# Kernel optimization log

Measured on AMD Instinct MI355X. Metric: run time of the kernel, lower is better.

## Reference

```python
import jax, jax.numpy as jnp
import numpy as np
from jax import lax

B, S, T = 32, 128, 128
V_SRC, V_TGT, E, U = 32000, 32000, 128, 256


def _lstm(xs, h0, c0, Wx, Wh, b):
    # xs: [T, B, F]; Keras gate order i, f, g(candidate), o
    def step(carry, x):
        h, c = carry
        z = x @ Wx + h @ Wh + b
        i, f, g, o = jnp.split(z, 4, axis=-1)
        c = jax.nn.sigmoid(f) * c + jax.nn.sigmoid(i) * jnp.tanh(g)
        h = jax.nn.sigmoid(o) * jnp.tanh(c)
        return (h, c), h
    (h, c), hs = lax.scan(step, (h0, c0), xs)
    return hs, h, c


def setup_inputs() -> dict:
    key = jax.random.key(0)
    ks = jax.random.split(key, 20)
    p = lambda k, shp: (jax.random.normal(k, shp, dtype=jnp.float32) * 0.02)
    return {
        "src": jax.random.randint(ks[0], (B, S), 0, V_SRC),
        "tgt": jax.random.randint(ks[1], (B, T), 0, V_TGT),
        "enc_emb": p(ks[2], (V_SRC, E)),
        "enc_Wx": p(ks[3], (E, 4 * U)),
        "enc_Wh": p(ks[4], (U, 4 * U)),
        "enc_b": jnp.zeros((4 * U,), jnp.float32),
        "dec_emb": p(ks[5], (V_TGT, E)),
        "dec_Wx": p(ks[6], (U + E, 4 * U)),
        "dec_Wh": p(ks[7], (U, 4 * U)),
        "dec_b": jnp.zeros((4 * U,), jnp.float32),
        "att_W1": p(ks[8], (U, U)),
        "att_b1": jnp.zeros((U,), jnp.float32),
        "att_W2": p(ks[9], (U, U)),
        "att_b2": jnp.zeros((U,), jnp.float32),
        "att_V": p(ks[10], (U, 1)),
        "att_bV": jnp.zeros((1,), jnp.float32),
        "fc_W": p(ks[11], (U, V_TGT)),
        "fc_b": jnp.zeros((V_TGT,), jnp.float32),
    }


def reference(src, tgt, enc_emb, enc_Wx, enc_Wh, enc_b, dec_emb, dec_Wx, dec_Wh,
              dec_b, att_W1, att_b1, att_W2, att_b2, att_V, att_bV, fc_W, fc_b):
    # ---- encoder ----
    enc_x = enc_emb[src]                                  # [B,S,E]
    enc_hs, h, c = _lstm(enc_x.transpose(1, 0, 2),
                         jnp.zeros((B, U), enc_Wx.dtype),
                         jnp.zeros((B, U), enc_Wx.dtype),
                         enc_Wx, enc_Wh, enc_b)
    enc_out = enc_hs.transpose(1, 0, 2)                   # [B,S,U]
    keys = enc_out @ att_W2 + att_b2                      # [B,S,U] (hoisted, same math)

    # ---- decoder (faithful: step 0 uses tgt[:,0]; step t>=1 uses tgt[:,t-1]) ----
    dec_tokens = jnp.concatenate([tgt[:, :1], tgt[:, :-1]], axis=1)  # [B,T]
    dec_x = dec_emb[dec_tokens].transpose(1, 0, 2)        # [T,B,E]

    def step(carry, x_emb):
        h, c = carry
        q = (h @ att_W1 + att_b1)[:, None, :]             # [B,1,U]
        score = jnp.tanh(q + keys) @ att_V + att_bV       # [B,S,1]
        attn = jax.nn.softmax(score, axis=1)
        ctx = jnp.sum(attn * enc_out, axis=1)             # [B,U]
        xin = jnp.concatenate([ctx, x_emb], axis=-1)      # [B,U+E]
        z = xin @ dec_Wx + h @ dec_Wh + dec_b
        i, f, g, o = jnp.split(z, 4, axis=-1)
        c = jax.nn.sigmoid(f) * c + jax.nn.sigmoid(i) * jnp.tanh(g)
        h = jax.nn.sigmoid(o) * jnp.tanh(c)
        probs = jax.nn.softmax(h @ fc_W + fc_b, axis=-1)  # [B,V]
        return (h, c), probs

    _, out = lax.scan(step, (h, c), dec_x)                # [T,B,V]
    return out.transpose(1, 0, 2)                         # [B,T,V]
```

## Files before the change

kernel.cpp:

```cpp
#include <hip/hip_runtime.h>
#include <hip/hip_bf16.h>
#include <hip/hip_fp16.h>
#include <cstdint>
#include <cstddef>

#define B_ 32
#define S_ 128
#define T_ 128
#define E_ 128
#define U_ 256
#define V_ 32000
#define G4 1024
#define TV 4096000

typedef __attribute__((ext_vector_type(8))) short short8_t;
typedef __attribute__((ext_vector_type(4))) float f32x4;
typedef unsigned long long u64;

static __device__ __forceinline__ unsigned short f2bf(float x) {
  union { float f; unsigned int u; } v; v.f = x;
  unsigned int r = (v.u + 0x7fffu + ((v.u >> 16) & 1u)) >> 16;
  return (unsigned short)r;
}
static __device__ __forceinline__ unsigned int pack2bf(float a, float b) {
  return (unsigned int)f2bf(a) | ((unsigned int)f2bf(b) << 16);
}
static __device__ __forceinline__ float bf_lo(unsigned int w) { return __uint_as_float(w << 16); }
static __device__ __forceinline__ float bf_hi(unsigned int w) { return __uint_as_float(w & 0xffff0000u); }
static __device__ __forceinline__ float sigmoidf_(float x) {
  return 1.0f / (1.0f + __expf(-x));
}
static __device__ __forceinline__ float tanhf_(float x) {
  float e = __expf(2.0f * x);
  return 1.0f - 2.0f / (e + 1.0f);
}

static __device__ __forceinline__ unsigned int f2e5(float x) {
  __half h = __float2half(x);
  __half_raw hr = *(__half_raw*)&h;
  unsigned int u = hr.x;
  unsigned int r = (u + 0x7Fu + ((u >> 8) & 1u)) >> 8;
  return r & 0xFFu;
}

static __device__ __forceinline__ unsigned pk2(float a, float b) {
  auto h = __builtin_amdgcn_cvt_pkrtz(a, b);
  return __builtin_bit_cast(unsigned, h);
}
#define SEL01 0x05000400u
#define SEL23 0x07000600u
static __device__ __forceinline__ unsigned e5pair(unsigned w, unsigned sel) {
  return __builtin_amdgcn_perm(w, 0u, sel);
}
static __device__ __forceinline__ float dot2(unsigned a, unsigned b, float c) {
  float d;
  asm("v_dot2_f32_f16 %0, %1, %2, %3" : "=v"(d) : "v"(a), "v"(b), "v"(c));
  return d;
}
static __device__ __forceinline__ unsigned pkadd(unsigned a, unsigned b) {
  unsigned d; asm("v_pk_add_f16 %0, %1, %2" : "=v"(d) : "v"(a), "v"(b)); return d;
}
static __device__ __forceinline__ unsigned pkmul(unsigned a, unsigned b) {
  unsigned d; asm("v_pk_mul_f16 %0, %1, %2" : "=v"(d) : "v"(a), "v"(b)); return d;
}
static __device__ __forceinline__ unsigned pkfma(unsigned a, unsigned b, unsigned c) {
  unsigned d; asm("v_pk_fma_f16 %0, %1, %2, %3" : "=v"(d) : "v"(a), "v"(b), "v"(c)); return d;
}
static __device__ __forceinline__ unsigned pkmax(unsigned a, unsigned b) {
  unsigned d; asm("v_pk_max_f16 %0, %1, %2" : "=v"(d) : "v"(a), "v"(b)); return d;
}
static __device__ __forceinline__ unsigned pkmin(unsigned a, unsigned b) {
  unsigned d; asm("v_pk_min_f16 %0, %1, %2" : "=v"(d) : "v"(a), "v"(b)); return d;
}

static __device__ __forceinline__ void pub64u(u64* p, unsigned val, unsigned tag) {
  u64 v = ((u64)tag << 32) | (u64)val;
  __hip_atomic_store(p, v, __ATOMIC_RELAXED, __HIP_MEMORY_SCOPE_AGENT);
}
static __device__ __forceinline__ void pub64(u64* p, float val, unsigned tag) {
  pub64u(p, __float_as_uint(val), tag);
}
static __device__ __forceinline__ u64 ld64(const u64* p) {
  return __hip_atomic_load(p, __ATOMIC_RELAXED, __HIP_MEMORY_SCOPE_AGENT);
}

__global__ __launch_bounds__(256) void k_prep_x(
    const int* __restrict__ src, const int* __restrict__ tgt,
    const float* __restrict__ enc_emb, const float* __restrict__ enc_Wx,
    const float* __restrict__ enc_b,
    const float* __restrict__ dec_emb, const float* __restrict__ dec_Wx,
    const float* __restrict__ dec_b,
    float* __restrict__ Xe, float* __restrict__ Xd)
{
  __shared__ float emb_l[8][E_];
  int wg = blockIdx.x;
  int tid = threadIdx.x;
  bool is_dec = (wg >= 512);
  int r0 = (is_dec ? (wg - 512) : wg) * 8;
  const float* emb  = is_dec ? dec_emb : enc_emb;
  const float* W    = is_dec ? (dec_Wx + (size_t)U_ * G4) : enc_Wx;
  const float* bias = is_dec ? dec_b : enc_b;
  float* Xout = is_dec ? Xd : Xe;

  for (int i = 0; i < 4; ++i) {
    int lin = i * 256 + tid;
    int rr = lin >> 7, k = lin & 127;
    int r = r0 + rr;
    int b = r & 31, st = r >> 5;
    int tok;
    if (is_dec) tok = tgt[b * T_ + (st > 0 ? st - 1 : 0)];
    else        tok = src[b * S_ + st];
    emb_l[rr][k] = emb[(size_t)tok * E_ + k];
  }
  __syncthreads();

  float acc[8][4];
  #pragma unroll
  for (int rr = 0; rr < 8; ++rr)
    #pragma unroll
    for (int cc = 0; cc < 4; ++cc) acc[rr][cc] = 0.f;

  for (int k = 0; k < E_; ++k) {
    float w0 = W[(size_t)k * G4 + tid];
    float w1 = W[(size_t)k * G4 + tid + 256];
    float w2 = W[(size_t)k * G4 + tid + 512];
    float w3 = W[(size_t)k * G4 + tid + 768];
    #pragma unroll
    for (int rr = 0; rr < 8; ++rr) {
      float e = emb_l[rr][k];
      acc[rr][0] += e * w0; acc[rr][1] += e * w1;
      acc[rr][2] += e * w2; acc[rr][3] += e * w3;
    }
  }
  #pragma unroll
  for (int rr = 0; rr < 8; ++rr) {
    int r = r0 + rr;
    #pragma unroll
    for (int cc = 0; cc < 4; ++cc) {
      int col = tid + cc * 256;
      Xout[(size_t)r * G4 + col] = acc[rr][cc] + bias[col];
    }
  }
}

__global__ __launch_bounds__(256) void k_prep_fcw(
    const float* __restrict__ fcW, unsigned short* __restrict__ fcWt)
{
  __shared__ float tile[64][65];
  int bid = blockIdx.x, tid = threadIdx.x;
  int n0 = (bid % 500) * 64, k0 = (bid / 500) * 64;
  for (int i = 0; i < 16; ++i) {
    int lin = i * 256 + tid;
    int k = lin >> 6, n = lin & 63;
    tile[k][n] = fcW[(size_t)(k0 + k) * V_ + n0 + n];
  }
  __syncthreads();
  for (int i = 0; i < 16; ++i) {
    int lin = i * 256 + tid;
    int n = lin >> 6, k = lin & 63;
    fcWt[(size_t)(n0 + n) * 256 + k0 + k] = f2bf(tile[k][n]);
  }
}

__global__ __launch_bounds__(256) void k_encoder8(
    const float* __restrict__ Xe, const float* __restrict__ Wh,
    float* __restrict__ enc_out, float* __restrict__ h_state,
    float* __restrict__ c_state, u64* __restrict__ hpubE )
{
  __shared__ unsigned int WhL[128][128];
  __shared__ float h_l[256];
  __shared__ float zp[2][128];

  int bid = blockIdx.x, tid = threadIdx.x;
  int g = bid & 7, b = bid >> 3;

  {
    int cl = tid & 127, kh = tid >> 7;
    int q = cl >> 5, r = cl & 31;
    int gc = q * 256 + g * 32 + r;
    for (int k2 = kh; k2 < 128; k2 += 2) {
      float w0 = Wh[(size_t)(2 * k2) * G4 + gc];
      float w1 = Wh[(size_t)(2 * k2 + 1) * G4 + gc];
      WhL[k2][cl] = pack2bf(w0, w1);
    }
  }
  float c_reg = 0.f, h_reg = 0.f;
  __syncthreads();

  for (int s = 0; s < S_; ++s) {
    if (s == 0) {
      h_l[tid] = 0.f;
    } else {
      const u64* p = &hpubE[((size_t)(s & 1) * 32 + b) * 256 + tid];
      u64 v = ld64(p);
      while ((unsigned)(v >> 32) < (unsigned)s) { __builtin_amdgcn_s_sleep(1); v = ld64(p); }
      h_l[tid] = __uint_as_float((unsigned)v);
    }
    __syncthreads();
    {
      int half = tid >> 7, cl = tid & 127;
      int k2b = half * 64;
      float a0 = 0.f, a1 = 0.f, a2 = 0.f, a3 = 0.f;
      #pragma unroll 4
      for (int k2 = 0; k2 < 64; k2 += 4) {
        unsigned w0 = WhL[k2b + k2][cl];
        unsigned w1 = WhL[k2b + k2 + 1][cl];
        unsigned w2 = WhL[k2b + k2 + 2][cl];
        unsigned w3 = WhL[k2b + k2 + 3][cl];
        a0 += h_l[2*(k2b+k2)]   * bf_lo(w0) + h_l[2*(k2b+k2)+1] * bf_hi(w0);
        a1 += h_l[2*(k2b+k2)+2] * bf_lo(w1) + h_l[2*(k2b+k2)+3] * bf_hi(w1);
        a2 += h_l[2*(k2b+k2)+4] * bf_lo(w2) + h_l[2*(k2b+k2)+5] * bf_hi(w2);
        a3 += h_l[2*(k2b+k2)+6] * bf_lo(w3) + h_l[2*(k2b+k2)+7] * bf_hi(w3);
      }
      zp[half][cl] = (a0 + a1) + (a2 + a3);
    }
    __syncthreads();
    if (tid < 32) {
      int r = tid, gc = g * 32 + r;
      const float* xe = Xe + (size_t)(s * B_ + b) * G4;
      float zi = zp[0][r]      + zp[1][r]      + xe[gc];
      float zf = zp[0][32 + r] + zp[1][32 + r] + xe[256 + gc];
      float zg = zp[0][64 + r] + zp[1][64 + r] + xe[512 + gc];
      float zo = zp[0][96 + r] + zp[1][96 + r] + xe[768 + gc];
      float c = sigmoidf_(zf) * c_reg + sigmoidf_(zi) * tanhf_(zg);
      c_reg = c;
      float h = sigmoidf_(zo) * tanhf_(c);
      h_reg = h;
      enc_out[((size_t)(b * S_ + s)) * U_ + gc] = h;
      pub64(&hpubE[((size_t)((s + 1) & 1) * 32 + b) * 256 + gc], h, (unsigned)(s + 1));
    }
  }
  if (tid < 32) {
    h_state[b * U_ + g * 32 + tid] = h_reg;
    c_state[b * U_ + g * 32 + tid] = c_reg;
  }
}

__global__ __launch_bounds__(256) void k_keys(
    const float* __restrict__ enc_out, const float* __restrict__ W2,
    const float* __restrict__ b2, float* __restrict__ keys)
{
  __shared__ float x_l[8][U_];
  int wg = blockIdx.x, tid = threadIdx.x;
  int r0 = wg * 8;
  for (int i = 0; i < 8; ++i) x_l[i][tid] = enc_out[(size_t)(r0 + i) * U_ + tid];
  __syncthreads();
  float acc[8];
  #pragma unroll
  for (int rr = 0; rr < 8; ++rr) acc[rr] = 0.f;
  for (int k = 0; k < U_; ++k) {
    float w = W2[(size_t)k * U_ + tid];
    #pragma unroll
    for (int rr = 0; rr < 8; ++rr) acc[rr] += x_l[rr][k] * w;
  }
  float bb = b2[tid];
  #pragma unroll
  for (int rr = 0; rr < 8; ++rr)
    keys[(size_t)(r0 + rr) * U_ + tid] = acc[rr] + bb;
}

__global__ __launch_bounds__(512) void k_decoder8(
    const float* __restrict__ Xd, const float* __restrict__ dec_Wx,
    const float* __restrict__ Wh,
    const float* __restrict__ W1, const float* __restrict__ b1,
    const float* __restrict__ attV, const float* __restrict__ attbV,
    const float* __restrict__ enc_out, const float* __restrict__ keys,
    const float* __restrict__ h0, const float* __restrict__ c0,
    unsigned short* __restrict__ Hbf,
    u64* __restrict__ hpub2 ,
    u64* __restrict__ qp2   )
{
  __shared__ unsigned int WxU[128 * 65];
  __shared__ unsigned int WhU[128 * 65];
  __shared__ unsigned int keyU[128 * 65];
  __shared__ unsigned int eoT[256 * 33];
  __shared__ unsigned int W1L[16][256];
  __shared__ unsigned int q2[160];
  __shared__ unsigned int aV2[160];
  __shared__ unsigned int b1p[128];
  __shared__ unsigned int h2[128];
  __shared__ unsigned int ctx2[128];
  __shared__ unsigned int esc2[64];
  __shared__ float escw[8];
  __shared__ float scr_c[512];
  __shared__ float scr_z[512];
  __shared__ float hsl[32];

  int bid = blockIdx.x, tid = threadIdx.x;
  int b = bid & 31, g = bid >> 5;
  int lane = tid & 63, wid = tid >> 6;

  for (int idx = tid; idx < 128 * 64; idx += 512) {
    int c = idx & 127, k4 = idx >> 7;
    int gc = ((c >> 5) << 8) + g * 32 + (c & 31);
    unsigned wx = 0, wh = 0;
    #pragma unroll
    for (int i = 0; i < 4; ++i) {
      int k = k4 * 4 + i;
      wx |= f2e5(dec_Wx[(size_t)k * G4 + gc]) << (8 * i);
      wh |= f2e5(Wh[(size_t)k * G4 + gc]) << (8 * i);
    }
    WxU[c * 65 + k4] = wx;
    WhU[c * 65 + k4] = wh;
  }
  for (int idx = tid; idx < 128 * 64; idx += 512) {
    int s = idx >> 6, u4 = idx & 63;
    float4 kv = *(const float4*)(keys + ((size_t)b * S_ + s) * U_ + u4 * 4);
    keyU[s * 65 + u4] = f2e5(kv.x) | (f2e5(kv.y) << 8) | (f2e5(kv.z) << 16) | (f2e5(kv.w) << 24);
  }
  for (int idx = tid; idx < 256 * 32; idx += 512) {
    int u = idx & 255, s4 = idx >> 8;
    unsigned w = 0;
    #pragma unroll
    for (int i = 0; i < 4; ++i) {
      int s = s4 * 4 + i;
      w |= f2e5(enc_out[((size_t)b * S_ + s) * U_ + u]) << (8 * i);
    }
    eoT[u * 33 + s4] = w;
  }
  if (tid < 256) {
    #pragma unroll
    for (int k2 = 0; k2 < 16; ++k2)
      W1L[k2][tid] = pk2(W1[(size_t)(g * 32 + 2 * k2) * U_ + tid],
                         W1[(size_t)(g * 32 + 2 * k2 + 1) * U_ + tid]);
  }
  if (tid < 128) {
    aV2[(tid >> 5) * 40 + (tid & 31)] = pk2(attV[2 * tid], attV[2 * tid + 1]);
    b1p[tid] = pk2(b1[2 * tid], b1[2 * tid + 1]);
  }
  float bV = attbV[0];
  float c_reg = 0.f, h_reg = 0.f;
  if (tid < 32) {
    h_reg = h0[b * U_ + g * 32 + tid];
    c_reg = c0[b * U_ + g * 32 + tid];
    hsl[tid] = h_reg;
  }
  __syncthreads();

  if (tid < 256) {
    float qp0 = 0.f, qp1 = 0.f;
    #pragma unroll
    for (int k2 = 0; k2 < 16; k2 += 2) {
      qp0 = dot2(W1L[k2][tid],     pk2(hsl[2*k2],   hsl[2*k2+1]), qp0);
      qp1 = dot2(W1L[k2+1][tid],   pk2(hsl[2*k2+2], hsl[2*k2+3]), qp1);
    }
    float qp = qp0 + qp1;
    float qpx = __shfl_xor(qp, 1);
    if (!(tid & 1))
      pub64u(&qp2[(((size_t)0 * 32 + b) * 128 + (tid >> 1)) * 8 + g], pk2(qp, qpx), 1u);
  }
  if (tid < 32) {
    float hx = __shfl_xor(h_reg, 1);
    if (!(tid & 1))
      pub64u(&hpub2[((size_t)0 * 32 + b) * 128 + g * 16 + (tid >> 1)], pk2(h_reg, hx), 1u);
  }

  const unsigned NEG1 = pk2(-1.f, -1.f), POS1 = pk2(1.f, 1.f);
  const unsigned C1 = pk2(-0.333333333f, -0.333333333f);
  const unsigned C2 = pk2(0.133333333f, 0.133333333f);
  const unsigned C3 = pk2(-0.053968254f, -0.053968254f);

  for (int t = 0; t < T_; ++t) {
    unsigned tag = (unsigned)(t + 1);
    int par = t & 1;

    float xd0 = 0.f, xd1 = 0.f, xd2 = 0.f, xd3 = 0.f;
    if (tid < 32) {
      const float* xd = Xd + (size_t)(t * B_ + b) * G4;
      int gc = g * 32 + tid;
      xd0 = xd[gc]; xd1 = xd[256 + gc]; xd2 = xd[512 + gc]; xd3 = xd[768 + gc];
    }

    if (tid < 128) {
      const u64* hp = &hpub2[((size_t)par * 32 + b) * 128 + tid];
      const u64* qp = &qp2[(((size_t)par * 32 + b) * 128 + tid) * 8];
      u64 vh, vq[8];
      bool ok;
      do {
        vh = ld64(hp);
        #pragma unroll
        for (int gg = 0; gg < 8; ++gg) vq[gg] = ld64(qp + gg);
        ok = ((unsigned)(vh >> 32) >= tag);
        #pragma unroll
        for (int gg = 0; gg < 8; ++gg) ok &= ((unsigned)(vq[gg] >> 32) >= tag);
        if (!ok) __builtin_amdgcn_s_sleep(1);
      } while (!ok);
      h2[tid] = (unsigned)vh;
      unsigned s0 = pkadd((unsigned)vq[0], (unsigned)vq[1]);
      unsigned s1 = pkadd((unsigned)vq[2], (unsigned)vq[3]);
      unsigned s2 = pkadd((unsigned)vq[4], (unsigned)vq[5]);
      unsigned s3 = pkadd((unsigned)vq[6], (unsigned)vq[7]);
      unsigned qs = pkadd(pkadd(s0, s1), pkadd(s2, s3));
      q2[(tid >> 5) * 40 + (tid & 31)] = pkadd(qs, b1p[tid]);
    }
    __syncthreads();

    {
      int s = tid >> 2, uq = tid & 3;
      const unsigned* kr = &keyU[s * 65 + uq * 16];
      const unsigned* qq = &q2[uq * 40];
      const unsigned* vv = &aV2[uq * 40];
      float a0 = 0.f, a1 = 0.f, a2 = 0.f, a3 = 0.f;
      #pragma unroll
      for (int j = 0; j < 16; j += 2) {
        unsigned w0 = kr[j], w1 = kr[j + 1];
        unsigned x0 = pkadd(e5pair(w0, SEL01), qq[2 * j]);
        unsigned x1 = pkadd(e5pair(w0, SEL23), qq[2 * j + 1]);
        unsigned x2 = pkadd(e5pair(w1, SEL01), qq[2 * j + 2]);
        unsigned x3 = pkadd(e5pair(w1, SEL23), qq[2 * j + 3]);
        x0 = pkmin(pkmax(x0, NEG1), POS1);
        x1 = pkmin(pkmax(x1, NEG1), POS1);
        x2 = pkmin(pkmax(x2, NEG1), POS1);
        x3 = pkmin(pkmax(x3, NEG1), POS1);
        unsigned s0_ = pkmul(x0, x0), s1_ = pkmul(x1, x1);
        unsigned s2_ = pkmul(x2, x2), s3_ = pkmul(x3, x3);
        unsigned t0 = pkfma(s0_, C3, C2), t1 = pkfma(s1_, C3, C2);
        unsigned t2 = pkfma(s2_, C3, C2), t3 = pkfma(s3_, C3, C2);
        t0 = pkfma(s0_, t0, C1); t1 = pkfma(s1_, t1, C1);
        t2 = pkfma(s2_, t2, C1); t3 = pkfma(s3_, t3, C1);
        unsigned th0 = pkfma(pkmul(x0, s0_), t0, x0);
        unsigned th1 = pkfma(pkmul(x1, s1_), t1, x1);
        unsigned th2 = pkfma(pkmul(x2, s2_), t2, x2);
        unsigned th3 = pkfma(pkmul(x3, s3_), t3, x3);
        a0 = dot2(th0, vv[2 * j], a0);
        a1 = dot2(th1, vv[2 * j + 1], a1);
        a2 = dot2(th2, vv[2 * j + 2], a2);
        a3 = dot2(th3, vv[2 * j + 3], a3);
      }
      float a = (a0 + a1) + (a2 + a3);
      a += __shfl_xor(a, 1); a += __shfl_xor(a, 2);
      float ea = __expf(a + bV);
      float ep = __shfl_xor(ea, 4);
      if (uq == 0 && !(s & 1)) esc2[s >> 1] = pk2(ea, ep);
      float dsum = ea;
      dsum += __shfl_xor(dsum, 4); dsum += __shfl_xor(dsum, 8);
      dsum += __shfl_xor(dsum, 16); dsum += __shfl_xor(dsum, 32);
      if (lane == 0) escw[wid] = dsum;
    }
    {
      int c = tid & 127, kq = tid >> 7;
      const unsigned* whp = &WhU[c * 65 + kq * 16];
      const unsigned* hh2 = &h2[kq * 32];
      float zb0 = 0.f, zb1 = 0.f;
      #pragma unroll
      for (int j = 0; j < 16; ++j) {
        unsigned wh = whp[j];
        zb0 = dot2(e5pair(wh, SEL01), hh2[2 * j], zb0);
        zb1 = dot2(e5pair(wh, SEL23), hh2[2 * j + 1], zb1);
      }
      scr_z[kq * 128 + c] = zb0 + zb1;
    }
    __syncthreads();

    {
      int u = tid & 255, sh = tid >> 8;
      const unsigned* ep = &eoT[u * 33 + sh * 16];
      const unsigned* e2 = &esc2[sh * 32];
      float c0a = 0.f, c1a = 0.f;
      #pragma unroll
      for (int j = 0; j < 16; ++j) {
        unsigned w = ep[j];
        c0a = dot2(e5pair(w, SEL01), e2[2 * j], c0a);
        c1a = dot2(e5pair(w, SEL23), e2[2 * j + 1], c1a);
      }
      scr_c[sh * 256 + u] = c0a + c1a;
    }
    __syncthreads();

    if (tid < 128) {
      float d = ((escw[0] + escw[1]) + (escw[2] + escw[3])) +
                ((escw[4] + escw[5]) + (escw[6] + escw[7]));
      float dinv = 1.0f / d;
      float ca = (scr_c[2 * tid]     + scr_c[256 + 2 * tid])     * dinv;
      float cb = (scr_c[2 * tid + 1] + scr_c[256 + 2 * tid + 1]) * dinv;
      ctx2[tid] = pk2(ca, cb);
    }
    __syncthreads();

    {
      int c = tid & 127, kq = tid >> 7;
      const unsigned* wxp = &WxU[c * 65 + kq * 16];
      const unsigned* cc2 = &ctx2[kq * 32];
      float za0 = 0.f, za1 = 0.f;
      #pragma unroll
      for (int j = 0; j < 16; ++j) {
        unsigned wx = wxp[j];
        za0 = dot2(e5pair(wx, SEL01), cc2[2 * j], za0);
        za1 = dot2(e5pair(wx, SEL23), cc2[2 * j + 1], za1);
      }
      scr_z[kq * 128 + c] += za0 + za1;
    }
    __syncthreads();

    int par1 = (t + 1) & 1;
    unsigned tag2 = (unsigned)(t + 2);
    if (tid < 32) {
      int r = tid, gc = g * 32 + r;
      float zi = scr_z[r]      + scr_z[128 + r]      + scr_z[256 + r]      + scr_z[384 + r]      + xd0;
      float zf = scr_z[32 + r] + scr_z[128 + 32 + r] + scr_z[256 + 32 + r] + scr_z[384 + 32 + r] + xd1;
      float zg = scr_z[64 + r] + scr_z[128 + 64 + r] + scr_z[256 + 64 + r] + scr_z[384 + 64 + r] + xd2;
      float zo = scr_z[96 + r] + scr_z[128 + 96 + r] + scr_z[256 + 96 + r] + scr_z[384 + 96 + r] + xd3;
      float c = sigmoidf_(zf) * c_reg + sigmoidf_(zi) * tanhf_(zg);
      c_reg = c;
      float h = sigmoidf_(zo) * tanhf_(c);
      h_reg = h;
      hsl[r] = h;
      Hbf[(size_t)(t * B_ + b) * U_ + gc] = f2bf(h);
      if (t < T_ - 1) {
        float hx = __shfl_xor(h, 1);
        if (!(r & 1))
          pub64u(&hpub2[((size_t)par1 * 32 + b) * 128 + g * 16 + (r >> 1)], pk2(h, hx), tag2);
      }
    }
    __syncthreads();

    if (t < T_ - 1 && tid < 256) {
      float qp0 = 0.f, qp1 = 0.f;
      #pragma unroll
      for (int k2 = 0; k2 < 16; k2 += 2) {
        qp0 = dot2(W1L[k2][tid],   pk2(hsl[2*k2],   hsl[2*k2+1]), qp0);
        qp1 = dot2(W1L[k2+1][tid], pk2(hsl[2*k2+2], hsl[2*k2+3]), qp1);
      }
      float qp = qp0 + qp1;
      float qpx = __shfl_xor(qp, 1);
      if (!(tid & 1))
        pub64u(&qp2[(((size_t)par1 * 32 + b) * 128 + (tid >> 1)) * 8 + g], pk2(qp, qpx), tag2);
    }
  }
}

__global__ __launch_bounds__(256) void k_fc(
    const unsigned short* __restrict__ Hbf, const unsigned short* __restrict__ fcWt,
    const float* __restrict__ fcb, float* __restrict__ out,
    float* __restrict__ rs_part)
{
  __shared__ uint4 Al[128 * 8];
  __shared__ uint4 Bl[128 * 8];
  __shared__ float rsum_l[128][2];

  int bid = blockIdx.x, tid = threadIdx.x;
  int nt = bid >> 5, mt = bid & 31;
  int m0 = mt * 128, n0 = nt * 128;
  int lane = tid & 63, wave = tid >> 6;
  int wm = (wave >> 1) * 64, wn = (wave & 1) * 64;
  int g = lane >> 4, r15 = lane & 15;

  f32x4 acc[4][4];
  f32x4 zero = {0.f, 0.f, 0.f, 0.f};
  #pragma unroll
  for (int mi = 0; mi < 4; ++mi)
    #pragma unroll
    for (int ni = 0; ni < 4; ++ni) acc[mi][ni] = zero;

  const unsigned short* Ag = Hbf  + (size_t)m0 * 256;
  const unsigned short* Bg = fcWt + (size_t)n0 * 256;

  for (int kt = 0; kt < 4; ++kt) {
    int kk = kt * 64;
    #pragma unroll
    for (int blk = 0; blk < 4; ++blk) {
      int lin = blk * 256 + tid;
      int row = lin >> 3, kq = lin & 7;
      Al[row * 8 + (kq ^ (row & 7))] = *(const uint4*)(Ag + (size_t)row * 256 + kk + kq * 8);
      Bl[row * 8 + (kq ^ (row & 7))] = *(const uint4*)(Bg + (size_t)row * 256 + kk + kq * 8);
    }
    __syncthreads();
    #pragma unroll
    for (int kk2 = 0; kk2 < 2; ++kk2) {
      short8_t a[4], bfr[4];
      #pragma unroll
      for (int mi = 0; mi < 4; ++mi) {
        int row = wm + mi * 16 + r15;
        a[mi] = *(const short8_t*)&Al[row * 8 + ((kk2 * 4 + g) ^ (row & 7))];
      }
      #pragma unroll
      for (int ni = 0; ni < 4; ++ni) {
        int row = wn + ni * 16 + r15;
        bfr[ni] = *(const short8_t*)&Bl[row * 8 + ((kk2 * 4 + g) ^ (row & 7))];
      }
      #pragma unroll
      for (int mi = 0; mi < 4; ++mi)
        #pragma unroll
        for (int ni = 0; ni < 4; ++ni)
          acc[mi][ni] = __builtin_amdgcn_mfma_f32_16x16x32_bf16(a[mi], bfr[ni], acc[mi][ni], 0, 0, 0);
    }
    __syncthreads();
  }

  float fcb_l[4];
  #pragma unroll
  for (int ni = 0; ni < 4; ++ni) fcb_l[ni] = fcb[n0 + wn + ni * 16 + r15];

  #pragma unroll
  for (int mi = 0; mi < 4; ++mi) {
    #pragma unroll
    for (int jj = 0; jj < 4; ++jj) {
      int rloc = wm + mi * 16 + g * 4 + jj;
      int grow = m0 + rloc;
      int bb = grow & 31, tt = grow >> 5;
      size_t obase = (size_t)bb * TV + (size_t)tt * V_;
      float s = 0.f;
      #pragma unroll
      for (int ni = 0; ni < 4; ++ni) {
        float v = __expf(acc[mi][ni][jj] + fcb_l[ni]);
        out[obase + n0 + wn + ni * 16 + r15] = v;
        s += v;
      }
      s += __shfl_xor(s, 1); s += __shfl_xor(s, 2);
      s += __shfl_xor(s, 4); s += __shfl_xor(s, 8);
      if (r15 == 0) rsum_l[rloc][wave & 1] = s;
    }
  }
  __syncthreads();
  if (tid < 128)
    rs_part[(size_t)nt * 4096 + m0 + tid] = rsum_l[tid][0] + rsum_l[tid][1];
}

__global__ __launch_bounds__(256) void k_rowsum(
    const float* __restrict__ rs_part, float* __restrict__ row_inv)
{
  int gidx = blockIdx.x * 256 + threadIdx.x;
  float s = 0.f;
  for (int nt = 0; nt < 250; ++nt) s += rs_part[(size_t)nt * 4096 + gidx];
  row_inv[gidx] = 1.0f / s;
}

__global__ __launch_bounds__(256) void k_norm(
    float4* __restrict__ out4, const float* __restrict__ row_inv)
{
  const long total = 32768000;
  long stride = (long)gridDim.x * 256;
  for (long i = (long)blockIdx.x * 256 + threadIdx.x; i < total; i += stride) {
    long flat = i * 4;
    int bb = (int)(flat / TV);
    int rem = (int)(flat % TV);
    int tt = rem / V_;
    float sc = row_inv[tt * 32 + bb];
    float4 v = out4[i];
    v.x *= sc; v.y *= sc; v.z *= sc; v.w *= sc;
    out4[i] = v;
  }
}

extern "C" void kernel_launch(void* const* d_in, const int* in_sizes, int n_in,
                              void* d_out, int out_size, void* d_ws, size_t ws_size,
                              hipStream_t stream) {
  (void)in_sizes; (void)n_in; (void)out_size; (void)ws_size;
  const int*   src     = (const int*)d_in[0];
  const int*   tgt     = (const int*)d_in[1];
  const float* enc_emb = (const float*)d_in[2];
  const float* enc_Wx  = (const float*)d_in[3];
  const float* enc_Wh  = (const float*)d_in[4];
  const float* enc_b   = (const float*)d_in[5];
  const float* dec_emb = (const float*)d_in[6];
  const float* dec_Wx  = (const float*)d_in[7];
  const float* dec_Wh  = (const float*)d_in[8];
  const float* dec_b   = (const float*)d_in[9];
  const float* att_W1  = (const float*)d_in[10];
  const float* att_b1  = (const float*)d_in[11];
  const float* att_W2  = (const float*)d_in[12];
  const float* att_b2  = (const float*)d_in[13];
  const float* att_V   = (const float*)d_in[14];
  const float* att_bV  = (const float*)d_in[15];
  const float* fc_W    = (const float*)d_in[16];
  const float* fc_b    = (const float*)d_in[17];
  float* out = (float*)d_out;

  char* ws = (char*)d_ws;
  size_t o = 0;
  auto alloc = [&](size_t bytes) {
    char* p = ws + o;
    o = (o + bytes + 255) & ~(size_t)255;
    return p;
  };
  float*          Xe      = (float*)alloc((size_t)S_ * B_ * G4 * 4);
  float*          Xd      = (float*)alloc((size_t)T_ * B_ * G4 * 4);
  float*          enc_out = (float*)alloc((size_t)B_ * S_ * U_ * 4);
  float*          keys    = (float*)alloc((size_t)B_ * S_ * U_ * 4);
  unsigned short* Hbf     = (unsigned short*)alloc((size_t)T_ * B_ * U_ * 2);
  unsigned short* fcWt    = (unsigned short*)alloc((size_t)V_ * U_ * 2);
  float*          h_state = (float*)alloc((size_t)B_ * U_ * 4);
  float*          c_state = (float*)alloc((size_t)B_ * U_ * 4);
  float*          rs_part = (float*)alloc((size_t)250 * 4096 * 4);
  float*          row_inv = (float*)alloc((size_t)4096 * 4);
  size_t pub_off = o;
  u64* hpubE = (u64*)alloc((size_t)2 * 32 * 256 * 8);
  u64* hpub2 = (u64*)alloc((size_t)2 * 32 * 128 * 8);
  u64* qp2   = (u64*)alloc((size_t)2 * 32 * 128 * 8 * 8);
  size_t pub_bytes = o - pub_off;

  hipMemsetAsync(ws + pub_off, 0, pub_bytes, stream);
  hipLaunchKernelGGL(k_prep_x, dim3(1024), dim3(256), 0, stream,
                     src, tgt, enc_emb, enc_Wx, enc_b, dec_emb, dec_Wx, dec_b, Xe, Xd);
  hipLaunchKernelGGL(k_prep_fcw, dim3(2000), dim3(256), 0, stream, fc_W, fcWt);
  hipLaunchKernelGGL(k_encoder8, dim3(256), dim3(256), 0, stream,
                     Xe, enc_Wh, enc_out, h_state, c_state, hpubE);
  hipLaunchKernelGGL(k_keys, dim3(512), dim3(256), 0, stream,
                     enc_out, att_W2, att_b2, keys);
  hipLaunchKernelGGL(k_decoder8, dim3(256), dim3(512), 0, stream,
                     Xd, dec_Wx, dec_Wh, att_W1, att_b1, att_V, att_bV,
                     enc_out, keys, h_state, c_state, Hbf,
                     hpub2, qp2);
  hipLaunchKernelGGL(k_fc, dim3(8000), dim3(256), 0, stream,
                     Hbf, fcWt, fc_b, out, rs_part);
  hipLaunchKernelGGL(k_rowsum, dim3(16), dim3(256), 0, stream, rs_part, row_inv);
  hipLaunchKernelGGL(k_norm, dim3(2048), dim3(256), 0, stream,
                     (float4*)d_out, row_inv);
}
```

Measured before the change: 1.511 ms.

## Split recurrent LSTMs across 4 workgroups per batch with 1024 threads and fp8 weights

Encoder and decoder recurrences now use 4 workgroups per batch row of 1024 threads each, instead of 8 workgroups of 256/512 threads. Fewer groups means fewer cross-workgroup handshakes per step. The encoder's Wh moves from bf16 to packed e5 (fp8) weights, and its published h becomes packed fp16 pairs. Keys and a transposed encoder output are pre-quantized to fp8 in k_keys, and the decoder streams them from global memory each step instead of holding them in LDS, which trades LDS capacity for repeated global/L2 reads and lower encoder precision.

```diff
diff --git a/kernel.cpp b/kernel.cpp
--- a/kernel.cpp
+++ b/kernel.cpp
@@ -22,11 +22,6 @@
   unsigned int r = (v.u + 0x7fffu + ((v.u >> 16) & 1u)) >> 16;
   return (unsigned short)r;
 }
-static __device__ __forceinline__ unsigned int pack2bf(float a, float b) {
-  return (unsigned int)f2bf(a) | ((unsigned int)f2bf(b) << 16);
-}
-static __device__ __forceinline__ float bf_lo(unsigned int w) { return __uint_as_float(w << 16); }
-static __device__ __forceinline__ float bf_hi(unsigned int w) { return __uint_as_float(w & 0xffff0000u); }
 static __device__ __forceinline__ float sigmoidf_(float x) {
   return 1.0f / (1.0f + __expf(-x));
 }
@@ -76,9 +71,6 @@
 static __device__ __forceinline__ void pub64u(u64* p, unsigned val, unsigned tag) {
   u64 v = ((u64)tag << 32) | (u64)val;
   __hip_atomic_store(p, v, __ATOMIC_RELAXED, __HIP_MEMORY_SCOPE_AGENT);
-}
-static __device__ __forceinline__ void pub64(u64* p, float val, unsigned tag) {
-  pub64u(p, __float_as_uint(val), tag);
 }
 static __device__ __forceinline__ u64 ld64(const u64* p) {
   return __hip_atomic_load(p, __ATOMIC_RELAXED, __HIP_MEMORY_SCOPE_AGENT);
@@ -162,83 +154,89 @@
   }
 }
 
-__global__ __launch_bounds__(256) void k_encoder8(
+__global__ __launch_bounds__(1024) void k_encoder4(
     const float* __restrict__ Xe, const float* __restrict__ Wh,
     float* __restrict__ enc_out, float* __restrict__ h_state,
     float* __restrict__ c_state, u64* __restrict__ hpubE )
 {
-  __shared__ unsigned int WhL[128][128];
-  __shared__ float h_l[256];
-  __shared__ float zp[2][128];
+  __shared__ unsigned int WhU[64 * 256];
+  __shared__ unsigned int h2[128];
+  __shared__ float scr_z[4 * 256];
 
   int bid = blockIdx.x, tid = threadIdx.x;
-  int g = bid & 7, b = bid >> 3;
-
-  {
-    int cl = tid & 127, kh = tid >> 7;
-    int q = cl >> 5, r = cl & 31;
-    int gc = q * 256 + g * 32 + r;
-    for (int k2 = kh; k2 < 128; k2 += 2) {
-      float w0 = Wh[(size_t)(2 * k2) * G4 + gc];
-      float w1 = Wh[(size_t)(2 * k2 + 1) * G4 + gc];
-      WhL[k2][cl] = pack2bf(w0, w1);
-    }
+  int b = bid & 31, g = bid >> 5;
+
+  for (int idx = tid; idx < 64 * 256; idx += 1024) {
+    int k4 = idx >> 8, c = idx & 255;
+    int gc = (c >> 6) * 256 + g * 64 + (c & 63);
+    unsigned w = 0;
+    #pragma unroll
+    for (int i = 0; i < 4; ++i)
+      w |= f2e5(Wh[(size_t)(4 * k4 + i) * G4 + gc]) << (8 * i);
+    WhU[k4 * 256 + c] = w;
   }
   float c_reg = 0.f, h_reg = 0.f;
   __syncthreads();
 
   for (int s = 0; s < S_; ++s) {
-    if (s == 0) {
-      h_l[tid] = 0.f;
-    } else {
-      const u64* p = &hpubE[((size_t)(s & 1) * 32 + b) * 256 + tid];
-      u64 v = ld64(p);
-      while ((unsigned)(v >> 32) < (unsigned)s) { __builtin_amdgcn_s_sleep(1); v = ld64(p); }
-      h_l[tid] = __uint_as_float((unsigned)v);
+    if (tid < 128) {
+      if (s == 0) h2[tid] = 0u;
+      else {
+        const u64* p = &hpubE[((size_t)(s & 1) * 32 + b) * 128 + tid];
+        u64 v = ld64(p);
+        while ((unsigned)(v >> 32) < (unsigned)s) { __builtin_amdgcn_s_sleep(1); v = ld64(p); }
+        h2[tid] = (unsigned)v;
+      }
     }
     __syncthreads();
     {
-      int half = tid >> 7, cl = tid & 127;
-      int k2b = half * 64;
-      float a0 = 0.f, a1 = 0.f, a2 = 0.f, a3 = 0.f;
-      #pragma unroll 4
-      for (int k2 = 0; k2 < 64; k2 += 4) {
-        unsigned w0 = WhL[k2b + k2][cl];
-        unsigned w1 = WhL[k2b + k2 + 1][cl];
-        unsigned w2 = WhL[k2b + k2 + 2][cl];
-        unsigned w3 = WhL[k2b + k2 + 3][cl];
-        a0 += h_l[2*(k2b+k2)]   * bf_lo(w0) + h_l[2*(k2b+k2)+1] * bf_hi(w0);
-        a1 += h_l[2*(k2b+k2)+2] * bf_lo(w1) + h_l[2*(k2b+k2)+3] * bf_hi(w1);
-        a2 += h_l[2*(k2b+k2)+4] * bf_lo(w2) + h_l[2*(k2b+k2)+5] * bf_hi(w2);
-        a3 += h_l[2*(k2b+k2)+6] * bf_lo(w3) + h_l[2*(k2b+k2)+7] * bf_hi(w3);
-      }
-      zp[half][cl] = (a0 + a1) + (a2 + a3);
-    }
-    __syncthreads();
-    if (tid < 32) {
-      int r = tid, gc = g * 32 + r;
+      int c = tid & 255, kq = tid >> 8;
+      const unsigned* wp = &WhU[(kq * 16) * 256 + c];
+      const unsigned* hh = &h2[kq * 32];
+      float z0 = 0.f, z1 = 0.f;
+      #pragma unroll
+      for (int j = 0; j < 16; ++j) {
+        unsigned w = wp[j * 256];
+        z0 = dot2(e5pair(w, SEL01), hh[2 * j], z0);
+        z1 = dot2(e5pair(w, SEL23), hh[2 * j + 1], z1);
+      }
+      scr_z[kq * 256 + c] = z0 + z1;
+    }
+    __syncthreads();
+    if (tid < 64) {
+      int r = tid, gc = g * 64 + r;
       const float* xe = Xe + (size_t)(s * B_ + b) * G4;
-      float zi = zp[0][r]      + zp[1][r]      + xe[gc];
-      float zf = zp[0][32 + r] + zp[1][32 + r] + xe[256 + gc];
-      float zg = zp[0][64 + r] + zp[1][64 + r] + xe[512 + gc];
-      float zo = zp[0][96 + r] + zp[1][96 + r] + xe[768 + gc];
-      float c = sigmoidf_(zf) * c_reg + sigmoidf_(zi) * tanhf_(zg);
+      float z[4];
+      #pragma unroll
+      for (int q = 0; q < 4; ++q) {
+        int c = q * 64 + r;
+        z[q] = scr_z[c] + scr_z[256 + c] + scr_z[512 + c] + scr_z[768 + c]
+             + xe[q * 256 + gc];
+      }
+      float c = sigmoidf_(z[1]) * c_reg + sigmoidf_(z[0]) * tanhf_(z[2]);
       c_reg = c;
-      float h = sigmoidf_(zo) * tanhf_(c);
+      float h = sigmoidf_(z[3]) * tanhf_(c);
       h_reg = h;
       enc_out[((size_t)(b * S_ + s)) * U_ + gc] = h;
-      pub64(&hpubE[((size_t)((s + 1) & 1) * 32 + b) * 256 + gc], h, (unsigned)(s + 1));
-    }
-  }
-  if (tid < 32) {
-    h_state[b * U_ + g * 32 + tid] = h_reg;
-    c_state[b * U_ + g * 32 + tid] = c_reg;
+      if (s < S_ - 1) {
+        float hx = __shfl_xor(h, 1);
+        if (!(r & 1))
+          pub64u(&hpubE[((size_t)((s + 1) & 1) * 32 + b) * 128 + g * 32 + (r >> 1)],
+                 pk2(h, hx), (unsigned)(s + 1));
+      }
+    }
+    __syncthreads();
+  }
+  if (tid < 64) {
+    h_state[b * U_ + g * 64 + tid] = h_reg;
+    c_state[b * U_ + g * 64 + tid] = c_reg;
   }
 }
 
 __global__ __launch_bounds__(256) void k_keys(
     const float* __restrict__ enc_out, const float* __restrict__ W2,
-    const float* __restrict__ b2, float* __restrict__ keys)
+    const float* __restrict__ b2,
+    unsigned char* __restrict__ keys8, unsigned char* __restrict__ eo8T)
 {
   __shared__ float x_l[8][U_];
   int wg = blockIdx.x, tid = threadIdx.x;
@@ -255,104 +253,94 @@
   }
   float bb = b2[tid];
   #pragma unroll
-  for (int rr = 0; rr < 8; ++rr)
-    keys[(size_t)(r0 + rr) * U_ + tid] = acc[rr] + bb;
-}
-
-__global__ __launch_bounds__(512) void k_decoder8(
+  for (int rr = 0; rr < 8; ++rr) {
+    int r = r0 + rr;
+    keys8[(size_t)r * U_ + tid] = (unsigned char)f2e5(acc[rr] + bb);
+    int bI = r >> 7, sI = r & 127;
+    eo8T[((size_t)bI * U_ + tid) * S_ + sI] = (unsigned char)f2e5(x_l[rr][tid]);
+  }
+}
+
+__global__ __launch_bounds__(1024) void k_decoder4(
     const float* __restrict__ Xd, const float* __restrict__ dec_Wx,
     const float* __restrict__ Wh,
     const float* __restrict__ W1, const float* __restrict__ b1,
     const float* __restrict__ attV, const float* __restrict__ attbV,
-    const float* __restrict__ enc_out, const float* __restrict__ keys,
+    const unsigned char* __restrict__ keys8, const unsigned char* __restrict__ eo8T,
     const float* __restrict__ h0, const float* __restrict__ c0,
     unsigned short* __restrict__ Hbf,
     u64* __restrict__ hpub2 ,
     u64* __restrict__ qp2   )
 {
-  __shared__ unsigned int WxU[128 * 65];
-  __shared__ unsigned int WhU[128 * 65];
-  __shared__ unsigned int keyU[128 * 65];
-  __shared__ unsigned int eoT[256 * 33];
-  __shared__ unsigned int W1L[16][256];
+  __shared__ unsigned int WxU[64 * 256];
+  __shared__ unsigned int WhU[64 * 256];
+  __shared__ unsigned int W1U[16 * 256];
+  __shared__ float scr_c[4 * 256];
+  __shared__ float scr_z[4 * 256];
   __shared__ unsigned int q2[160];
   __shared__ unsigned int aV2[160];
   __shared__ unsigned int b1p[128];
   __shared__ unsigned int h2[128];
   __shared__ unsigned int ctx2[128];
   __shared__ unsigned int esc2[64];
-  __shared__ float escw[8];
-  __shared__ float scr_c[512];
-  __shared__ float scr_z[512];
-  __shared__ float hsl[32];
+  __shared__ float escw[16];
+  __shared__ float hsl[64];
 
   int bid = blockIdx.x, tid = threadIdx.x;
   int b = bid & 31, g = bid >> 5;
   int lane = tid & 63, wid = tid >> 6;
 
-  for (int idx = tid; idx < 128 * 64; idx += 512) {
-    int c = idx & 127, k4 = idx >> 7;
-    int gc = ((c >> 5) << 8) + g * 32 + (c & 31);
+  for (int idx = tid; idx < 64 * 256; idx += 1024) {
+    int k4 = idx >> 8, c = idx & 255;
+    int gc = (c >> 6) * 256 + g * 64 + (c & 63);
     unsigned wx = 0, wh = 0;
     #pragma unroll
     for (int i = 0; i < 4; ++i) {
-      int k = k4 * 4 + i;
+      int k = 4 * k4 + i;
       wx |= f2e5(dec_Wx[(size_t)k * G4 + gc]) << (8 * i);
       wh |= f2e5(Wh[(size_t)k * G4 + gc]) << (8 * i);
     }
-    WxU[c * 65 + k4] = wx;
-    WhU[c * 65 + k4] = wh;
-  }
-  for (int idx = tid; idx < 128 * 64; idx += 512) {
-    int s = idx >> 6, u4 = idx & 63;
-    float4 kv = *(const float4*)(keys + ((size_t)b * S_ + s) * U_ + u4 * 4);
-    keyU[s * 65 + u4] = f2e5(kv.x) | (f2e5(kv.y) << 8) | (f2e5(kv.z) << 16) | (f2e5(kv.w) << 24);
-  }
-  for (int idx = tid; idx < 256 * 32; idx += 512) {
-    int u = idx & 255, s4 = idx >> 8;
+    WxU[k4 * 256 + c] = wx;
+    WhU[k4 * 256 + c] = wh;
+  }
+  for (int idx = tid; idx < 16 * 256; idx += 1024) {
+    int k4 = idx >> 8, u = idx & 255;
     unsigned w = 0;
     #pragma unroll
-    for (int i = 0; i < 4; ++i) {
-      int s = s4 * 4 + i;
-      w |= f2e5(enc_out[((size_t)b * S_ + s) * U_ + u]) << (8 * i);
-    }
-    eoT[u * 33 + s4] = w;
-  }
-  if (tid < 256) {
-    #pragma unroll
-    for (int k2 = 0; k2 < 16; ++k2)
-      W1L[k2][tid] = pk2(W1[(size_t)(g * 32 + 2 * k2) * U_ + tid],
-                         W1[(size_t)(g * 32 + 2 * k2 + 1) * U_ + tid]);
+    for (int i = 0; i < 4; ++i)
+      w |= f2e5(W1[(size_t)(g * 64 + 4 * k4 + i) * U_ + u]) << (8 * i);
+    W1U[k4 * 256 + u] = w;
   }
   if (tid < 128) {
-    aV2[(tid >> 5) * 40 + (tid & 31)] = pk2(attV[2 * tid], attV[2 * tid + 1]);
+    aV2[(tid >> 4) * 20 + (tid & 15)] = pk2(attV[2 * tid], attV[2 * tid + 1]);
     b1p[tid] = pk2(b1[2 * tid], b1[2 * tid + 1]);
   }
   float bV = attbV[0];
   float c_reg = 0.f, h_reg = 0.f;
-  if (tid < 32) {
-    h_reg = h0[b * U_ + g * 32 + tid];
-    c_reg = c0[b * U_ + g * 32 + tid];
+  if (tid < 64) {
+    h_reg = h0[b * U_ + g * 64 + tid];
+    c_reg = c0[b * U_ + g * 64 + tid];
     hsl[tid] = h_reg;
   }
   __syncthreads();
 
   if (tid < 256) {
-    float qp0 = 0.f, qp1 = 0.f;
-    #pragma unroll
-    for (int k2 = 0; k2 < 16; k2 += 2) {
-      qp0 = dot2(W1L[k2][tid],     pk2(hsl[2*k2],   hsl[2*k2+1]), qp0);
-      qp1 = dot2(W1L[k2+1][tid],   pk2(hsl[2*k2+2], hsl[2*k2+3]), qp1);
-    }
-    float qp = qp0 + qp1;
+    float qa = 0.f, qb = 0.f;
+    #pragma unroll
+    for (int j = 0; j < 16; ++j) {
+      unsigned w = W1U[j * 256 + tid];
+      qa = dot2(e5pair(w, SEL01), pk2(hsl[4 * j],     hsl[4 * j + 1]), qa);
+      qb = dot2(e5pair(w, SEL23), pk2(hsl[4 * j + 2], hsl[4 * j + 3]), qb);
+    }
+    float qp = qa + qb;
     float qpx = __shfl_xor(qp, 1);
     if (!(tid & 1))
-      pub64u(&qp2[(((size_t)0 * 32 + b) * 128 + (tid >> 1)) * 8 + g], pk2(qp, qpx), 1u);
-  }
-  if (tid < 32) {
+      pub64u(&qp2[(((size_t)0 * 32 + b) * 128 + (tid >> 1)) * 4 + g], pk2(qp, qpx), 1u);
+  }
+  if (tid < 64) {
     float hx = __shfl_xor(h_reg, 1);
     if (!(tid & 1))
-      pub64u(&hpub2[((size_t)0 * 32 + b) * 128 + g * 16 + (tid >> 1)], pk2(h_reg, hx), 1u);
+      pub64u(&hpub2[((size_t)0 * 32 + b) * 128 + g * 32 + (tid >> 1)], pk2(h_reg, hx), 1u);
   }
 
   const unsigned NEG1 = pk2(-1.f, -1.f), POS1 = pk2(1.f, 1.f);
@@ -360,171 +348,172 @@
   const unsigned C2 = pk2(0.133333333f, 0.133333333f);
   const unsigned C3 = pk2(-0.053968254f, -0.053968254f);
 
+  const unsigned char* kb = keys8 + (size_t)b * S_ * U_;
+  const unsigned char* eb = eo8T + (size_t)b * U_ * S_;
+
   for (int t = 0; t < T_; ++t) {
     unsigned tag = (unsigned)(t + 1);
     int par = t & 1;
 
     float xd0 = 0.f, xd1 = 0.f, xd2 = 0.f, xd3 = 0.f;
-    if (tid < 32) {
-      const float* xd = Xd + (size_t)(t * B_ + b) * G4;
-      int gc = g * 32 + tid;
-      xd0 = xd[gc]; xd1 = xd[256 + gc]; xd2 = xd[512 + gc]; xd3 = xd[768 + gc];
+    if (tid < 64) {
+      const float* xd = Xd + (size_t)(t * B_ + b) * G4 + g * 64 + tid;
+      xd0 = xd[0]; xd1 = xd[256]; xd2 = xd[512]; xd3 = xd[768];
     }
 
     if (tid < 128) {
       const u64* hp = &hpub2[((size_t)par * 32 + b) * 128 + tid];
-      const u64* qp = &qp2[(((size_t)par * 32 + b) * 128 + tid) * 8];
-      u64 vh, vq[8];
+      const u64* qp = &qp2[(((size_t)par * 32 + b) * 128 + tid) * 4];
+      u64 vh, v0, v1, v2, v3;
       bool ok;
       do {
         vh = ld64(hp);
-        #pragma unroll
-        for (int gg = 0; gg < 8; ++gg) vq[gg] = ld64(qp + gg);
-        ok = ((unsigned)(vh >> 32) >= tag);
-        #pragma unroll
-        for (int gg = 0; gg < 8; ++gg) ok &= ((unsigned)(vq[gg] >> 32) >= tag);
+        v0 = ld64(qp); v1 = ld64(qp + 1); v2 = ld64(qp + 2); v3 = ld64(qp + 3);
+        ok = ((unsigned)(vh >> 32) >= tag) & ((unsigned)(v0 >> 32) >= tag) &
+             ((unsigned)(v1 >> 32) >= tag) & ((unsigned)(v2 >> 32) >= tag) &
+             ((unsigned)(v3 >> 32) >= tag);
         if (!ok) __builtin_amdgcn_s_sleep(1);
       } while (!ok);
       h2[tid] = (unsigned)vh;
-      unsigned s0 = pkadd((unsigned)vq[0], (unsigned)vq[1]);
-      unsigned s1 = pkadd((unsigned)vq[2], (unsigned)vq[3]);
-      unsigned s2 = pkadd((unsigned)vq[4], (unsigned)vq[5]);
-      unsigned s3 = pkadd((unsigned)vq[6], (unsigned)vq[7]);
-      unsigned qs = pkadd(pkadd(s0, s1), pkadd(s2, s3));
-      q2[(tid >> 5) * 40 + (tid & 31)] = pkadd(qs, b1p[tid]);
-    }
-    __syncthreads();
-
+      unsigned qs = pkadd(pkadd((unsigned)v0, (unsigned)v1),
+                          pkadd((unsigned)v2, (unsigned)v3));
+      q2[(tid >> 4) * 20 + (tid & 15)] = pkadd(qs, b1p[tid]);
+    }
+    __syncthreads();
+
+    int sI = tid >> 3, uo = tid & 7;
+    int uI = tid & 255, sq = tid >> 8;
+    uint4 kw0, kw1, ew0, ew1;
     {
-      int s = tid >> 2, uq = tid & 3;
-      const unsigned* kr = &keyU[s * 65 + uq * 16];
-      const unsigned* qq = &q2[uq * 40];
-      const unsigned* vv = &aV2[uq * 40];
-      float a0 = 0.f, a1 = 0.f, a2 = 0.f, a3 = 0.f;
-      #pragma unroll
-      for (int j = 0; j < 16; j += 2) {
-        unsigned w0 = kr[j], w1 = kr[j + 1];
-        unsigned x0 = pkadd(e5pair(w0, SEL01), qq[2 * j]);
-        unsigned x1 = pkadd(e5pair(w0, SEL23), qq[2 * j + 1]);
-        unsigned x2 = pkadd(e5pair(w1, SEL01), qq[2 * j + 2]);
-        unsigned x3 = pkadd(e5pair(w1, SEL23), qq[2 * j + 3]);
+      const uint4* kp = (const uint4*)(kb + (size_t)sI * U_ + uo * 32);
+      kw0 = kp[0]; kw1 = kp[1];
+      const uint4* ep = (const uint4*)(eb + (size_t)uI * S_ + sq * 32);
+      ew0 = ep[0]; ew1 = ep[1];
+    }
+    float zreg;
+    {
+      int c = tid & 255, kq = tid >> 8;
+      const unsigned* wp = &WhU[(kq * 16) * 256 + c];
+      const unsigned* hh = &h2[kq * 32];
+      float z0 = 0.f, z1 = 0.f;
+      #pragma unroll
+      for (int j = 0; j < 16; ++j) {
+        unsigned w = wp[j * 256];
+        z0 = dot2(e5pair(w, SEL01), hh[2 * j], z0);
+        z1 = dot2(e5pair(w, SEL23), hh[2 * j + 1], z1);
+      }
+      zreg = z0 + z1;
+    }
+    {
+      unsigned kw[8] = {kw0.x, kw0.y, kw0.z, kw0.w, kw1.x, kw1.y, kw1.z, kw1.w};
+      const unsigned* qq = &q2[uo * 20];
+      const unsigned* vv = &aV2[uo * 20];
+      float a0 = 0.f, a1 = 0.f;
+      #pragma unroll
+      for (int j = 0; j < 8; ++j) {
+        unsigned w = kw[j];
+        unsigned x0 = pkadd(e5pair(w, SEL01), qq[2 * j]);
+        unsigned x1 = pkadd(e5pair(w, SEL23), qq[2 * j + 1]);
         x0 = pkmin(pkmax(x0, NEG1), POS1);
         x1 = pkmin(pkmax(x1, NEG1), POS1);
-        x2 = pkmin(pkmax(x2, NEG1), POS1);
-        x3 = pkmin(pkmax(x3, NEG1), POS1);
         unsigned s0_ = pkmul(x0, x0), s1_ = pkmul(x1, x1);
-        unsigned s2_ = pkmul(x2, x2), s3_ = pkmul(x3, x3);
         unsigned t0 = pkfma(s0_, C3, C2), t1 = pkfma(s1_, C3, C2);
-        unsigned t2 = pkfma(s2_, C3, C2), t3 = pkfma(s3_, C3, C2);
         t0 = pkfma(s0_, t0, C1); t1 = pkfma(s1_, t1, C1);
-        t2 = pkfma(s2_, t2, C1); t3 = pkfma(s3_, t3, C1);
         unsigned th0 = pkfma(pkmul(x0, s0_), t0, x0);
         unsigned th1 = pkfma(pkmul(x1, s1_), t1, x1);
-        unsigned th2 = pkfma(pkmul(x2, s2_), t2, x2);
-        unsigned th3 = pkfma(pkmul(x3, s3_), t3, x3);
         a0 = dot2(th0, vv[2 * j], a0);
         a1 = dot2(th1, vv[2 * j + 1], a1);
-        a2 = dot2(th2, vv[2 * j + 2], a2);
-        a3 = dot2(th3, vv[2 * j + 3], a3);
-      }
-      float a = (a0 + a1) + (a2 + a3);
-      a += __shfl_xor(a, 1); a += __shfl_xor(a, 2);
+      }
+      float a = a0 + a1;
+      a += __shfl_xor(a, 1); a += __shfl_xor(a, 2); a += __shfl_xor(a, 4);
       float ea = __expf(a + bV);
-      float ep = __shfl_xor(ea, 4);
-      if (uq == 0 && !(s & 1)) esc2[s >> 1] = pk2(ea, ep);
+      float ep = __shfl_xor(ea, 8);
+      if (uo == 0 && !(sI & 1)) esc2[sI >> 1] = pk2(ea, ep);
       float dsum = ea;
-      dsum += __shfl_xor(dsum, 4); dsum += __shfl_xor(dsum, 8);
-      dsum += __shfl_xor(dsum, 16); dsum += __shfl_xor(dsum, 32);
+      dsum += __shfl_xor(dsum, 8); dsum += __shfl_xor(dsum, 16); dsum += __shfl_xor(dsum, 32);
       if (lane == 0) escw[wid] = dsum;
     }
+    __syncthreads();
+
     {
-      int c = tid & 127, kq = tid >> 7;
-      const unsigned* whp = &WhU[c * 65 + kq * 16];
-      const unsigned* hh2 = &h2[kq * 32];
-      float zb0 = 0.f, zb1 = 0.f;
-      #pragma unroll
-      for (int j = 0; j < 16; ++j) {
-        unsigned wh = whp[j];
-        zb0 = dot2(e5pair(wh, SEL01), hh2[2 * j], zb0);
-        zb1 = dot2(e5pair(wh, SEL23), hh2[2 * j + 1], zb1);
-      }
-      scr_z[kq * 128 + c] = zb0 + zb1;
-    }
-    __syncthreads();
-
-    {
-      int u = tid & 255, sh = tid >> 8;
-      const unsigned* ep = &eoT[u * 33 + sh * 16];
-      const unsigned* e2 = &esc2[sh * 32];
+      unsigned ewv[8] = {ew0.x, ew0.y, ew0.z, ew0.w, ew1.x, ew1.y, ew1.z, ew1.w};
+      const unsigned* e2 = &esc2[sq * 16];
       float c0a = 0.f, c1a = 0.f;
       #pragma unroll
-      for (int j = 0; j < 16; ++j) {
-        unsigned w = ep[j];
+      for (int j = 0; j < 8; ++j) {
+        unsigned w = ewv[j];
         c0a = dot2(e5pair(w, SEL01), e2[2 * j], c0a);
         c1a = dot2(e5pair(w, SEL23), e2[2 * j + 1], c1a);
       }
-      scr_c[sh * 256 + u] = c0a + c1a;
+      scr_c[sq * 256 + uI] = c0a + c1a;
     }
     __syncthreads();
 
     if (tid < 128) {
       float d = ((escw[0] + escw[1]) + (escw[2] + escw[3])) +
-                ((escw[4] + escw[5]) + (escw[6] + escw[7]));
+                ((escw[4] + escw[5]) + (escw[6] + escw[7])) +
+                ((escw[8] + escw[9]) + (escw[10] + escw[11])) +
+                ((escw[12] + escw[13]) + (escw[14] + escw[15]));
       float dinv = 1.0f / d;
-      float ca = (scr_c[2 * tid]     + scr_c[256 + 2 * tid])     * dinv;
-      float cb = (scr_c[2 * tid + 1] + scr_c[256 + 2 * tid + 1]) * dinv;
+      int u0 = 2 * tid;
+      float ca = (scr_c[u0] + scr_c[256 + u0] + scr_c[512 + u0] + scr_c[768 + u0]) * dinv;
+      float cb = (scr_c[u0 + 1] + scr_c[256 + u0 + 1] + scr_c[512 + u0 + 1] + scr_c[768 + u0 + 1]) * dinv;
       ctx2[tid] = pk2(ca, cb);
     }
     __syncthreads();
 
     {
-      int c = tid & 127, kq = tid >> 7;
-      const unsigned* wxp = &WxU[c * 65 + kq * 16];
-      const unsigned* cc2 = &ctx2[kq * 32];
-      float za0 = 0.f, za1 = 0.f;
+      int c = tid & 255, kq = tid >> 8;
+      const unsigned* wp = &WxU[(kq * 16) * 256 + c];
+      const unsigned* cc = &ctx2[kq * 32];
+      float z0 = 0.f, z1 = 0.f;
       #pragma unroll
       for (int j = 0; j < 16; ++j) {
-        unsigned wx = wxp[j];
-        za0 = dot2(e5pair(wx, SEL01), cc2[2 * j], za0);
-        za1 = dot2(e5pair(wx, SEL23), cc2[2 * j + 1], za1);
-      }
-      scr_z[kq * 128 + c] += za0 + za1;
+        unsigned w = wp[j * 256];
+        z0 = dot2(e5pair(w, SEL01), cc[2 * j], z0);
+        z1 = dot2(e5pair(w, SEL23), cc[2 * j + 1], z1);
+      }
+      scr_z[kq * 256 + c] = zreg + z0 + z1;
     }
     __syncthreads();
 
     int par1 = (t + 1) & 1;
     unsigned tag2 = (unsigned)(t + 2);
-    if (tid < 32) {
-      int r = tid, gc = g * 32 + r;
-      float zi = scr_z[r]      + scr_z[128 + r]      + scr_z[256 + r]      + scr_z[384 + r]      + xd0;
-      float zf = scr_z[32 + r] + scr_z[128 + 32 + r] + scr_z[256 + 32 + r] + scr_z[384 + 32 + r] + xd1;
-      float zg = scr_z[64 + r] + scr_z[128 + 64 + r] + scr_z[256 + 64 + r] + scr_z[384 + 64 + r] + xd2;
-      float zo = scr_z[96 + r] + scr_z[128 + 96 + r] + scr_z[256 + 96 + r] + scr_z[384 + 96 + r] + xd3;
-      float c = sigmoidf_(zf) * c_reg + sigmoidf_(zi) * tanhf_(zg);
+    if (tid < 64) {
+      int r = tid, gc = g * 64 + r;
+      float z[4];
+      #pragma unroll
+      for (int q = 0; q < 4; ++q) {
+        int c = q * 64 + r;
+        z[q] = scr_z[c] + scr_z[256 + c] + scr_z[512 + c] + scr_z[768 + c];
+      }
+      z[0] += xd0; z[1] += xd1; z[2] += xd2; z[3] += xd3;
+      float c = sigmoidf_(z[1]) * c_reg + sigmoidf_(z[0]) * tanhf_(z[2]);
       c_reg = c;
-      float h = sigmoidf_(zo) * tanhf_(c);
+      float h = sigmoidf_(z[3]) * tanhf_(c);
       h_reg = h;
       hsl[r] = h;
       Hbf[(size_t)(t * B_ + b) * U_ + gc] = f2bf(h);
       if (t < T_ - 1) {
         float hx = __shfl_xor(h, 1);
         if (!(r & 1))
-          pub64u(&hpub2[((size_t)par1 * 32 + b) * 128 + g * 16 + (r >> 1)], pk2(h, hx), tag2);
+          pub64u(&hpub2[((size_t)par1 * 32 + b) * 128 + g * 32 + (r >> 1)], pk2(h, hx), tag2);
       }
     }
     __syncthreads();
 
     if (t < T_ - 1 && tid < 256) {
-      float qp0 = 0.f, qp1 = 0.f;
-      #pragma unroll
-      for (int k2 = 0; k2 < 16; k2 += 2) {
-        qp0 = dot2(W1L[k2][tid],   pk2(hsl[2*k2],   hsl[2*k2+1]), qp0);
-        qp1 = dot2(W1L[k2+1][tid], pk2(hsl[2*k2+2], hsl[2*k2+3]), qp1);
-      }
-      float qp = qp0 + qp1;
+      float qa = 0.f, qb = 0.f;
+      #pragma unroll
+      for (int j = 0; j < 16; ++j) {
+        unsigned w = W1U[j * 256 + tid];
+        qa = dot2(e5pair(w, SEL01), pk2(hsl[4 * j],     hsl[4 * j + 1]), qa);
+        qb = dot2(e5pair(w, SEL23), pk2(hsl[4 * j + 2], hsl[4 * j + 3]), qb);
+      }
+      float qp = qa + qb;
       float qpx = __shfl_xor(qp, 1);
       if (!(tid & 1))
-        pub64u(&qp2[(((size_t)par1 * 32 + b) * 128 + (tid >> 1)) * 8 + g], pk2(qp, qpx), tag2);
+        pub64u(&qp2[(((size_t)par1 * 32 + b) * 128 + (tid >> 1)) * 4 + g], pk2(qp, qpx), tag2);
     }
   }
 }
@@ -676,7 +665,8 @@
   float*          Xe      = (float*)alloc((size_t)S_ * B_ * G4 * 4);
   float*          Xd      = (float*)alloc((size_t)T_ * B_ * G4 * 4);
   float*          enc_out = (float*)alloc((size_t)B_ * S_ * U_ * 4);
-  float*          keys    = (float*)alloc((size_t)B_ * S_ * U_ * 4);
+  unsigned char*  keys8   = (unsigned char*)alloc((size_t)B_ * S_ * U_);
+  unsigned char*  eo8T    = (unsigned char*)alloc((size_t)B_ * U_ * S_);
   unsigned short* Hbf     = (unsigned short*)alloc((size_t)T_ * B_ * U_ * 2);
   unsigned short* fcWt    = (unsigned short*)alloc((size_t)V_ * U_ * 2);
   float*          h_state = (float*)alloc((size_t)B_ * U_ * 4);
@@ -684,22 +674,22 @@
   float*          rs_part = (float*)alloc((size_t)250 * 4096 * 4);
   float*          row_inv = (float*)alloc((size_t)4096 * 4);
   size_t pub_off = o;
-  u64* hpubE = (u64*)alloc((size_t)2 * 32 * 256 * 8);
+  u64* hpubE = (u64*)alloc((size_t)2 * 32 * 128 * 8);
   u64* hpub2 = (u64*)alloc((size_t)2 * 32 * 128 * 8);
-  u64* qp2   = (u64*)alloc((size_t)2 * 32 * 128 * 8 * 8);
+  u64* qp2   = (u64*)alloc((size_t)2 * 32 * 128 * 4 * 8);
   size_t pub_bytes = o - pub_off;
 
   hipMemsetAsync(ws + pub_off, 0, pub_bytes, stream);
   hipLaunchKernelGGL(k_prep_x, dim3(1024), dim3(256), 0, stream,
                      src, tgt, enc_emb, enc_Wx, enc_b, dec_emb, dec_Wx, dec_b, Xe, Xd);
   hipLaunchKernelGGL(k_prep_fcw, dim3(2000), dim3(256), 0, stream, fc_W, fcWt);
-  hipLaunchKernelGGL(k_encoder8, dim3(256), dim3(256), 0, stream,
+  hipLaunchKernelGGL(k_encoder4, dim3(128), dim3(1024), 0, stream,
                      Xe, enc_Wh, enc_out, h_state, c_state, hpubE);
   hipLaunchKernelGGL(k_keys, dim3(512), dim3(256), 0, stream,
-                     enc_out, att_W2, att_b2, keys);
-  hipLaunchKernelGGL(k_decoder8, dim3(256), dim3(512), 0, stream,
+                     enc_out, att_W2, att_b2, keys8, eo8T);
+  hipLaunchKernelGGL(k_decoder4, dim3(128), dim3(1024), 0, stream,
                      Xd, dec_Wx, dec_Wh, att_W1, att_b1, att_V, att_bV,
-                     enc_out, keys, h_state, c_state, Hbf,
+                     keys8, eo8T, h_state, c_state, Hbf,
                      hpub2, qp2);
   hipLaunchKernelGGL(k_fc, dim3(8000), dim3(256), 0, stream,
                      Hbf, fcWt, fc_b, out, rs_part);
```

After: 1.540 ms. About the same (+1.9%).
